# Kernel optimization log

Hardware: AMD Instinct MI355X
Metric: run time of the kernel (lower is better)

## Reference

```python
import jax, jax.numpy as jnp
import numpy as np

B, S = 2, 2048
NUM_HEADS, NUM_KV_HEADS, HEAD_DIM = 32, 8, 128
HIDDEN = NUM_HEADS * HEAD_DIM  # 4096
Q_SIZE = NUM_HEADS * HEAD_DIM
KV_SIZE = NUM_KV_HEADS * HEAD_DIM
ROPE_THETA = 100000.0
SCALE = HEAD_DIM ** -0.5


def setup_inputs() -> dict:
    key = jax.random.key(0)
    k1, k2, k3, k4, k5 = jax.random.split(key, 5)
    T = B * S
    return {
        "hidden_states": jax.random.normal(k1, (T, HIDDEN), jnp.float32) * 0.02,
        "positions": jnp.arange(T, dtype=jnp.int64) % S,  # per-sequence positions
        "w_qkv": jax.random.normal(k2, (HIDDEN, Q_SIZE + 2 * KV_SIZE), jnp.float32) * 0.02,
        "b_qkv": jax.random.normal(k3, (Q_SIZE + 2 * KV_SIZE,), jnp.float32) * 0.01,
        "w_o": jax.random.normal(k4, (Q_SIZE, HIDDEN), jnp.float32) * 0.02,
        "b_o": jax.random.normal(k5, (HIDDEN,), jnp.float32) * 0.01,
    }


def _rope_neox(x, positions):
    # x: [T, H, D]; neox style rotates the two halves of head_dim
    half = HEAD_DIM // 2
    inv_freq = 1.0 / (ROPE_THETA ** (jnp.arange(0, HEAD_DIM, 2, dtype=jnp.float32) / HEAD_DIM))
    freqs = positions.astype(jnp.float32)[:, None] * inv_freq[None, :]  # [T, D/2]
    cos = jnp.cos(freqs)[:, None, :]  # [T, 1, D/2]
    sin = jnp.sin(freqs)[:, None, :]
    x1, x2 = x[..., :half], x[..., half:]
    return jnp.concatenate([x1 * cos - x2 * sin, x2 * cos + x1 * sin], axis=-1)


def reference(hidden_states, positions, w_qkv, b_qkv, w_o, b_o):
    T = hidden_states.shape[0]
    qkv = hidden_states @ w_qkv + b_qkv  # [T, q+2kv]
    q = qkv[:, :Q_SIZE].reshape(T, NUM_HEADS, HEAD_DIM)
    k = qkv[:, Q_SIZE:Q_SIZE + KV_SIZE].reshape(T, NUM_KV_HEADS, HEAD_DIM)
    v = qkv[:, Q_SIZE + KV_SIZE:].reshape(T, NUM_KV_HEADS, HEAD_DIM)

    q = _rope_neox(q, positions)
    k = _rope_neox(k, positions)

    # reshape flattened tokens back to [B, S, ...] for causal self-attention
    q = q.reshape(B, S, NUM_HEADS, HEAD_DIM)
    k = k.reshape(B, S, NUM_KV_HEADS, HEAD_DIM)
    v = v.reshape(B, S, NUM_KV_HEADS, HEAD_DIM)

    # GQA: repeat kv heads to match query heads
    group = NUM_HEADS // NUM_KV_HEADS
    k = jnp.repeat(k, group, axis=2)  # [B, S, H, D]
    v = jnp.repeat(v, group, axis=2)

    scores = jnp.einsum("bqhd,bkhd->bhqk", q, k) * SCALE  # [B, H, S, S]
    causal = jnp.tril(jnp.ones((S, S), dtype=bool))
    scores = jnp.where(causal[None, None], scores, jnp.finfo(scores.dtype).min)
    probs = jax.nn.softmax(scores, axis=-1)
    attn = jnp.einsum("bhqk,bkhd->bqhd", probs, v)  # [B, S, H, D]

    attn = attn.reshape(T, Q_SIZE)
    return attn @ w_o + b_o  # [T, HIDDEN]
```

## Files before the change

kernel.cpp:

```cpp
#include <hip/hip_runtime.h>
#include <cstdint>
#include <math.h>

#define T_TOTAL 4096
#define S_LEN   2048
#define NH      32
#define NKV     8
#define HD      128
#define HIDDEN  4096
#define QSZ     4096
#define KVSZ    1024
#define QKV_N   6144
#define SCALE_F 0.08838834764831843f

typedef __bf16 bf16x8 __attribute__((ext_vector_type(8)));
typedef float  f32x4  __attribute__((ext_vector_type(4)));
typedef unsigned short u16;
typedef unsigned int   u32;
typedef u16 u16x8 __attribute__((ext_vector_type(8)));
typedef u16 u16x4 __attribute__((ext_vector_type(4)));

__device__ __forceinline__ u16 f2bf(float f) {
  u32 b = __float_as_uint(f);
  b += 0x7FFFu + ((b >> 16) & 1u);
  return (u16)(b >> 16);
}

__device__ __forceinline__ void async_copy16(const u16* g, u16* l) {
  __builtin_amdgcn_global_load_lds(
      (const __attribute__((address_space(1))) void*)(g),
      (__attribute__((address_space(3))) void*)(l), 16, 0, 0);
}

__global__ __launch_bounds__(256) void cast_bf16_kernel(const float4* __restrict__ in,
                                                        ushort4* __restrict__ out, int n4) {
  int i = blockIdx.x * 256 + threadIdx.x;
  if (i >= n4) return;
  float4 v = in[i];
  ushort4 o;
  o.x = f2bf(v.x); o.y = f2bf(v.y); o.z = f2bf(v.z); o.w = f2bf(v.w);
  out[i] = o;
}

__global__ __launch_bounds__(256) void transpose_cast_kernel(const float* __restrict__ in,
                                                             u16* __restrict__ out, int R, int C) {
  __shared__ float tile[32][33];
  int bx = blockIdx.x * 32;
  int by = blockIdx.y * 32;
  int tx = threadIdx.x & 31, ty = threadIdx.x >> 5;
  for (int i = ty; i < 32; i += 8)
    tile[i][tx] = in[(size_t)(by + i) * C + bx + tx];
  __syncthreads();
  for (int i = ty; i < 32; i += 8)
    out[(size_t)(bx + i) * R + by + tx] = f2bf(tile[tx][i]);
}

__global__ __launch_bounds__(512) void gemm_pipe_kernel(const u16* __restrict__ A,
                                                        const u16* __restrict__ Bt,
                                                        const float* __restrict__ bias,
                                                        float* __restrict__ C,
                                                        int M, int N, int K, int nbn) {
  __shared__ u16 lds[2][2][8192];
  const int tid  = threadIdx.x;
  const int lane = tid & 63, wave = tid >> 6;
  const int quad = lane >> 4, l16 = lane & 15;
  const int wm = (wave >> 2) * 128;
  const int wn = (wave & 3) * 64;

  const int cpx = gridDim.x >> 3;
  const int logical = (blockIdx.x & 7) * cpx + (blockIdx.x >> 3);
  const int bm = logical / nbn, bn = logical % nbn;

  const int trow = tid >> 2;
  const int gch  = ((tid & 3) ^ ((tid >> 3) & 3)) * 8;
  const u16* gA = A  + (size_t)(bm * 256 + trow) * K + gch;
  const u16* gB = Bt + (size_t)(bn * 256 + trow) * K + gch;
  const size_t eoff = (size_t)128 * K;

  const int NT = K >> 5;
#pragma unroll
  for (int pt = 0; pt < 2; ++pt) {
    int kt = pt * 32;
    async_copy16(gA + kt,        &lds[pt][0][tid * 8]);
    async_copy16(gA + eoff + kt, &lds[pt][0][4096 + tid * 8]);
    async_copy16(gB + kt,        &lds[pt][1][tid * 8]);
    async_copy16(gB + eoff + kt, &lds[pt][1][4096 + tid * 8]);
  }

  const int sw = (quad ^ ((l16 >> 1) & 3)) * 8;
  f32x4 acc[8][4] = {};
  for (int t = 0; t < NT; ++t) {
    if (t + 1 < NT) asm volatile("s_waitcnt vmcnt(4)" ::: "memory");
    else            asm volatile("s_waitcnt vmcnt(0)" ::: "memory");
    __builtin_amdgcn_s_barrier();

    const u16* sAt = lds[t & 1][0];
    const u16* sBt = lds[t & 1][1];
    bf16x8 af[8], bfr[4];
#pragma unroll
    for (int i = 0; i < 8; ++i)
      af[i] = *(const bf16x8*)&sAt[(wm + i * 16 + l16) * 32 + sw];
#pragma unroll
    for (int j = 0; j < 4; ++j)
      bfr[j] = *(const bf16x8*)&sBt[(wn + j * 16 + l16) * 32 + sw];
    asm volatile("s_waitcnt lgkmcnt(0)" ::: "memory");
    __builtin_amdgcn_s_barrier();

    if (t + 2 < NT) {
      int kt = (t + 2) * 32;
      async_copy16(gA + kt,        &lds[t & 1][0][tid * 8]);
      async_copy16(gA + eoff + kt, &lds[t & 1][0][4096 + tid * 8]);
      async_copy16(gB + kt,        &lds[t & 1][1][tid * 8]);
      async_copy16(gB + eoff + kt, &lds[t & 1][1][4096 + tid * 8]);
    }

    __builtin_amdgcn_s_setprio(1);
#pragma unroll
    for (int i = 0; i < 8; ++i)
#pragma unroll
      for (int j = 0; j < 4; ++j)
        acc[i][j] = __builtin_amdgcn_mfma_f32_16x16x32_bf16(af[i], bfr[j], acc[i][j], 0, 0, 0);
    __builtin_amdgcn_s_setprio(0);
  }

#pragma unroll
  for (int i = 0; i < 8; ++i) {
    int row0 = bm * 256 + wm + i * 16 + quad * 4;
#pragma unroll
    for (int j = 0; j < 4; ++j) {
      int col = bn * 256 + wn + j * 16 + l16;
      float bi = bias[col];
#pragma unroll
      for (int r = 0; r < 4; ++r)
        C[(size_t)(row0 + r) * N + col] = acc[i][j][r] + bi;
    }
  }
}

__global__ __launch_bounds__(256) void qk_rope_cast_kernel(const float* __restrict__ qkv,
                                                           const int* __restrict__ pos,
                                                           u16* __restrict__ Qb,
                                                           u16* __restrict__ Kb) {
  int idx = blockIdx.x * 256 + threadIdx.x;
  int t = idx / 2560;
  int rem = idx - t * 2560;
  int head = rem >> 6, i = rem & 63;
  int b = t >> 11, s = t & 2047;
  float p = (float)pos[t];
  float inv = exp2f(-(float)i * 0.25952563f);
  float f = p * inv;
  float sn, cs;
  sincosf(f, &sn, &cs);
  if (head < NH) {
    const float* src = qkv + (size_t)t * QKV_N + head * HD;
    float x1 = src[i], x2 = src[i + 64];
    u16* dst = Qb + (((size_t)(b * NH + head)) * S_LEN + s) * HD;
    dst[i]      = f2bf((x1 * cs - x2 * sn) * SCALE_F);
    dst[i + 64] = f2bf((x2 * cs + x1 * sn) * SCALE_F);
  } else {
    int kh = head - NH;
    const float* src = qkv + (size_t)t * QKV_N + QSZ + kh * HD;
    float x1 = src[i], x2 = src[i + 64];
    u16* dst = Kb + (((size_t)(b * NKV + kh)) * S_LEN + s) * HD;
    dst[i]      = f2bf(x1 * cs - x2 * sn);
    dst[i + 64] = f2bf(x2 * cs + x1 * sn);
  }
}

__global__ __launch_bounds__(256) void v_transpose_cast_kernel(const float* __restrict__ qkv,
                                                               u16* __restrict__ Vtb) {
  __shared__ float tile[32][33];
  int st = blockIdx.x * 32;
  int dt = blockIdx.y * 32;
  int bk = blockIdx.z;
  int b = bk >> 3, kvh = bk & 7;
  int tx = threadIdx.x & 31, ty = threadIdx.x >> 5;
  const float* src = qkv + (size_t)(b * S_LEN) * QKV_N + QSZ + KVSZ + kvh * HD;
  for (int i = ty; i < 32; i += 8)
    tile[i][tx] = src[(size_t)(st + i) * QKV_N + dt + tx];
  __syncthreads();
  u16* dst = Vtb + (size_t)bk * HD * S_LEN;
  for (int i = ty; i < 32; i += 8)
    dst[(size_t)(dt + i) * S_LEN + st + tx] = f2bf(tile[tx][i]);
}

__global__ __launch_bounds__(512) void flash_mfma_kernel(const u16* __restrict__ Qb,
                                                         const u16* __restrict__ Kb,
                                                         const u16* __restrict__ Vtb,
                                                         u16* __restrict__ attn) {
  const int qti = gridDim.x - 1 - blockIdx.x;
  const int h = blockIdx.y, b = blockIdx.z;
  const int kvh = h >> 2;
  const int tid = threadIdx.x;
  const int lane = tid & 63, wave = tid >> 6;
  const int quad = lane >> 4, l16 = lane & 15;

  __shared__ u16 smem[24576];
  u16* sK  = smem;
  u16* sVt = smem + 8192;
  u16* sPw = smem + 16384 + wave * 1024;

  bf16x8 qf[4];
  {
    const u16* qrow = Qb + (((size_t)(b * NH + h)) * S_LEN + (size_t)qti * 128 + wave * 16 + l16) * HD;
#pragma unroll
    for (int kc = 0; kc < 4; ++kc)
      qf[kc] = *(const bf16x8*)(qrow + kc * 32 + quad * 8);
  }

  f32x4 acc[8] = {};
  float m_r = -INFINITY;
  float l_r = 0.f;

  const u16* Kbase = Kb  + ((size_t)(b * NKV + kvh)) * S_LEN * HD;
  const u16* Vbase = Vtb + ((size_t)(b * NKV + kvh)) * HD * S_LEN;

  u16x8 kv[2], vv[2];
#pragma unroll
  for (int i = 0; i < 2; ++i) {
    int c = i * 512 + tid;
    kv[i] = *(const u16x8*)(Kbase + (size_t)(c >> 4) * HD + (c & 15) * 8);
    vv[i] = *(const u16x8*)(Vbase + (size_t)(c >> 3) * S_LEN + (c & 7) * 8);
  }

  const int nkt = 2 * qti + 2;
  const int lastkt = 2 * qti + (wave >> 2);

  for (int kt = 0; kt < nkt; ++kt) {
    __syncthreads();
#pragma unroll
    for (int i = 0; i < 2; ++i) {
      int c = i * 512 + tid;
      int kr = c >> 4;
      *(u16x8*)&sK[(kr * 128 + (c & 15) * 8) ^ ((kr & 7) << 3)] = kv[i];
      int vr = c >> 3;
      *(u16x8*)&sVt[(vr * 64 + (c & 7) * 8) ^ ((vr & 7) << 3)] = vv[i];
    }
    __syncthreads();

    if (kt + 1 < nkt) {
#pragma unroll
      for (int i = 0; i < 2; ++i) {
        int c = i * 512 + tid;
        kv[i] = *(const u16x8*)(Kbase + (size_t)((kt + 1) * 64 + (c >> 4)) * HD + (c & 15) * 8);
        vv[i] = *(const u16x8*)(Vbase + (size_t)(c >> 3) * S_LEN + (kt + 1) * 64 + (c & 7) * 8);
      }
    }

    if (kt > lastkt) continue;

    f32x4 s[4] = {};
#pragma unroll
    for (int kc = 0; kc < 4; ++kc) {
#pragma unroll
      for (int nb = 0; nb < 4; ++nb) {
        bf16x8 kf = *(const bf16x8*)&sK[((nb * 16 + l16) * 128 + kc * 32 + quad * 8) ^ ((l16 & 7) << 3)];
        s[nb] = __builtin_amdgcn_mfma_f32_16x16x32_bf16(kf, qf[kc], s[nb], 0, 0, 0);
      }
    }

    if (kt == lastkt) {
      int qg = qti * 128 + wave * 16 + l16;
      int k0 = kt * 64;
#pragma unroll
      for (int nb = 0; nb < 4; ++nb)
#pragma unroll
        for (int r = 0; r < 4; ++r)
          if (k0 + nb * 16 + quad * 4 + r > qg) s[nb][r] = -1e30f;
    }

    float mx = -1e30f;
#pragma unroll
    for (int nb = 0; nb < 4; ++nb)
#pragma unroll
      for (int r = 0; r < 4; ++r)
        mx = fmaxf(mx, s[nb][r]);
    float alpha = 1.f;
    if (!__all(mx - m_r <= 8.f)) {
      mx = fmaxf(mx, __shfl_xor(mx, 16));
      mx = fmaxf(mx, __shfl_xor(mx, 32));
      float mnew = fmaxf(m_r, mx);
      alpha = __expf(m_r - mnew);
      m_r = mnew;
#pragma unroll
      for (int db = 0; db < 8; ++db)
#pragma unroll
        for (int r = 0; r < 4; ++r)
          acc[db][r] *= alpha;
    }
    float rs = 0.f;
#pragma unroll
    for (int nb = 0; nb < 4; ++nb)
#pragma unroll
      for (int r = 0; r < 4; ++r) {
        float p = __expf(s[nb][r] - m_r);
        s[nb][r] = p;
        rs += p;
      }
    rs += __shfl_xor(rs, 16);
    rs += __shfl_xor(rs, 32);
    l_r = l_r * alpha + rs;

#pragma unroll
    for (int nb = 0; nb < 4; ++nb) {
      u16x4 pk;
#pragma unroll
      for (int r = 0; r < 4; ++r) pk[r] = f2bf(s[nb][r]);
      *(u16x4*)&sPw[(l16 * 64 + nb * 16 + quad * 4) ^ ((l16 & 7) << 3)] = pk;
    }

#pragma unroll
    for (int ch = 0; ch < 2; ++ch) {
      bf16x8 pf = *(const bf16x8*)&sPw[(l16 * 64 + ch * 32 + quad * 8) ^ ((l16 & 7) << 3)];
#pragma unroll
      for (int db = 0; db < 8; ++db) {
        bf16x8 vf = *(const bf16x8*)&sVt[((db * 16 + l16) * 64 + ch * 32 + quad * 8) ^ ((l16 & 7) << 3)];
        acc[db] = __builtin_amdgcn_mfma_f32_16x16x32_bf16(vf, pf, acc[db], 0, 0, 0);
      }
    }
  }

  float invl = 1.0f / l_r;
  __syncthreads();
  u16* sOw = &smem[wave * 2048];
#pragma unroll
  for (int db = 0; db < 8; ++db) {
    u16x4 pk;
#pragma unroll
    for (int r = 0; r < 4; ++r) pk[r] = f2bf(acc[db][r] * invl);
    *(u16x4*)&sOw[(l16 * 128 + db * 16 + quad * 4) ^ ((l16 & 7) << 3)] = pk;
  }
#pragma unroll
  for (int p = 0; p < 4; ++p) {
    int row = p * 4 + quad;
    u16x8 o = *(const u16x8*)&sOw[(row * 128 + l16 * 8) ^ ((row & 7) << 3)];
    int q = qti * 128 + wave * 16 + row;
    *(u16x8*)(attn + ((size_t)(b * S_LEN + q)) * QSZ + (size_t)h * HD + l16 * 8) = o;
  }
}

extern "C" void kernel_launch(void* const* d_in, const int* in_sizes, int n_in,
                              void* d_out, int out_size, void* d_ws, size_t ws_size,
                              hipStream_t stream) {
  const float* hidden    = (const float*)d_in[0];
  const int*   positions = (const int*)d_in[1];
  const float* w_qkv     = (const float*)d_in[2];
  const float* b_qkv     = (const float*)d_in[3];
  const float* w_o       = (const float*)d_in[4];
  const float* b_o       = (const float*)d_in[5];
  float* out = (float*)d_out;

  char* ws = (char*)d_ws;
  const size_t MB = 1024 * 1024;
  u16*   hb    = (u16*)ws;
  u16*   wqT   = (u16*)(ws + 32  * MB);
  u16*   woT   = (u16*)(ws + 80  * MB);
  float* qkv   = (float*)(ws + 112 * MB);
  u16*   attnb = (u16*)(ws + 208 * MB);
  u16*   Qb    = (u16*)ws;
  u16*   Kb    = (u16*)(ws + 32 * MB);
  u16*   Vtb   = (u16*)(ws + 40 * MB);

  cast_bf16_kernel<<<T_TOTAL * HIDDEN / 4 / 256, 256, 0, stream>>>(
      (const float4*)hidden, (ushort4*)hb, T_TOTAL * HIDDEN / 4);
  transpose_cast_kernel<<<dim3(QKV_N / 32, HIDDEN / 32), 256, 0, stream>>>(w_qkv, wqT, HIDDEN, QKV_N);
  transpose_cast_kernel<<<dim3(HIDDEN / 32, QSZ / 32), 256, 0, stream>>>(w_o, woT, QSZ, HIDDEN);
  gemm_pipe_kernel<<<dim3((T_TOTAL / 256) * (QKV_N / 256)), 512, 0, stream>>>(
      hb, wqT, b_qkv, qkv, T_TOTAL, QKV_N, HIDDEN, QKV_N / 256);
  qk_rope_cast_kernel<<<T_TOTAL * 2560 / 256, 256, 0, stream>>>(qkv, positions, Qb, Kb);
  v_transpose_cast_kernel<<<dim3(S_LEN / 32, HD / 32, 16), 256, 0, stream>>>(qkv, Vtb);
  flash_mfma_kernel<<<dim3(S_LEN / 128, NH, 2), 512, 0, stream>>>(Qb, Kb, Vtb, attnb);
  gemm_pipe_kernel<<<dim3((T_TOTAL / 256) * (HIDDEN / 256)), 512, 0, stream>>>(
      attnb, woT, b_o, out, T_TOTAL, HIDDEN, QSZ, HIDDEN / 256);
}
```

Baseline: 887.7 us.

## Shrink GEMM M-tile to 128 and use triple-buffered LDS with single barrier

The GEMM block tile goes from 256x256 to 128x256, which doubles the number of blocks so more CUs get work (the QKV GEMM had 384 blocks and the output GEMM 256). LDS is now a three-stage ring, so the prefetch for tile t+2 can be issued right after the first barrier, and the second per-iteration barrier is removed. In exchange, arithmetic intensity per block is lower because each B tile is reused for half as many rows, so L2 and global traffic go up.

Measured after the change: 887.6 us. No clear change (-0.0%).

```diff
diff --git a/kernel.cpp b/kernel.cpp
--- a/kernel.cpp
+++ b/kernel.cpp
@@ -60,72 +60,72 @@
                                                         const float* __restrict__ bias,
                                                         float* __restrict__ C,
                                                         int M, int N, int K, int nbn) {
-  __shared__ u16 lds[2][2][8192];
+  __shared__ u16 lds[3][12288];
   const int tid  = threadIdx.x;
   const int lane = tid & 63, wave = tid >> 6;
   const int quad = lane >> 4, l16 = lane & 15;
-  const int wm = (wave >> 2) * 128;
+  const int wm = (wave >> 2) * 64;
   const int wn = (wave & 3) * 64;
 
   const int cpx = gridDim.x >> 3;
   const int logical = (blockIdx.x & 7) * cpx + (blockIdx.x >> 3);
   const int bm = logical / nbn, bn = logical % nbn;
 
-  const int trow = tid >> 2;
-  const int gch  = ((tid & 3) ^ ((tid >> 3) & 3)) * 8;
-  const u16* gA = A  + (size_t)(bm * 256 + trow) * K + gch;
-  const u16* gB = Bt + (size_t)(bn * 256 + trow) * K + gch;
-  const size_t eoff = (size_t)128 * K;
+  const int gch = ((tid & 3) ^ ((tid >> 3) & 3)) * 8;
+  const u16* gA  = A  + (size_t)(bm * 128 + (tid >> 2)) * K + gch;
+  const u16* gB0 = Bt + (size_t)(bn * 256 + (tid >> 2)) * K + gch;
+  const u16* gB1 = gB0 + (size_t)128 * K;
 
   const int NT = K >> 5;
 #pragma unroll
   for (int pt = 0; pt < 2; ++pt) {
     int kt = pt * 32;
-    async_copy16(gA + kt,        &lds[pt][0][tid * 8]);
-    async_copy16(gA + eoff + kt, &lds[pt][0][4096 + tid * 8]);
-    async_copy16(gB + kt,        &lds[pt][1][tid * 8]);
-    async_copy16(gB + eoff + kt, &lds[pt][1][4096 + tid * 8]);
+    async_copy16(gA  + kt, &lds[pt][tid * 8]);
+    async_copy16(gB0 + kt, &lds[pt][4096 + tid * 8]);
+    async_copy16(gB1 + kt, &lds[pt][8192 + tid * 8]);
   }
 
   const int sw = (quad ^ ((l16 >> 1) & 3)) * 8;
-  f32x4 acc[8][4] = {};
+  f32x4 acc[4][4] = {};
+  int sl = 0;
   for (int t = 0; t < NT; ++t) {
-    if (t + 1 < NT) asm volatile("s_waitcnt vmcnt(4)" ::: "memory");
+    if (t + 1 < NT) asm volatile("s_waitcnt vmcnt(3)" ::: "memory");
     else            asm volatile("s_waitcnt vmcnt(0)" ::: "memory");
     __builtin_amdgcn_s_barrier();
 
-    const u16* sAt = lds[t & 1][0];
-    const u16* sBt = lds[t & 1][1];
-    bf16x8 af[8], bfr[4];
-#pragma unroll
-    for (int i = 0; i < 8; ++i)
+    int s2 = (sl == 0) ? 2 : sl - 1;
+    if (t + 2 < NT) {
+      int kt = (t + 2) * 32;
+      async_copy16(gA  + kt, &lds[s2][tid * 8]);
+      async_copy16(gB0 + kt, &lds[s2][4096 + tid * 8]);
+      async_copy16(gB1 + kt, &lds[s2][8192 + tid * 8]);
+    }
+
+    const u16* sAt = lds[sl];
+    const u16* sBt = &lds[sl][4096];
+    bf16x8 af[4], bfr[4];
+#pragma unroll
+    for (int i = 0; i < 4; ++i)
       af[i] = *(const bf16x8*)&sAt[(wm + i * 16 + l16) * 32 + sw];
 #pragma unroll
     for (int j = 0; j < 4; ++j)
       bfr[j] = *(const bf16x8*)&sBt[(wn + j * 16 + l16) * 32 + sw];
     asm volatile("s_waitcnt lgkmcnt(0)" ::: "memory");
-    __builtin_amdgcn_s_barrier();
-
-    if (t + 2 < NT) {
-      int kt = (t + 2) * 32;
-      async_copy16(gA + kt,        &lds[t & 1][0][tid * 8]);
-      async_copy16(gA + eoff + kt, &lds[t & 1][0][4096 + tid * 8]);
-      async_copy16(gB + kt,        &lds[t & 1][1][tid * 8]);
-      async_copy16(gB + eoff + kt, &lds[t & 1][1][4096 + tid * 8]);
-    }
 
     __builtin_amdgcn_s_setprio(1);
 #pragma unroll
-    for (int i = 0; i < 8; ++i)
+    for (int i = 0; i < 4; ++i)
 #pragma unroll
       for (int j = 0; j < 4; ++j)
         acc[i][j] = __builtin_amdgcn_mfma_f32_16x16x32_bf16(af[i], bfr[j], acc[i][j], 0, 0, 0);
     __builtin_amdgcn_s_setprio(0);
-  }
-
-#pragma unroll
-  for (int i = 0; i < 8; ++i) {
-    int row0 = bm * 256 + wm + i * 16 + quad * 4;
+
+    sl = (sl == 2) ? 0 : sl + 1;
+  }
+
+#pragma unroll
+  for (int i = 0; i < 4; ++i) {
+    int row0 = bm * 128 + wm + i * 16 + quad * 4;
 #pragma unroll
     for (int j = 0; j < 4; ++j) {
       int col = bn * 256 + wn + j * 16 + l16;
@@ -365,11 +365,11 @@
       (const float4*)hidden, (ushort4*)hb, T_TOTAL * HIDDEN / 4);
   transpose_cast_kernel<<<dim3(QKV_N / 32, HIDDEN / 32), 256, 0, stream>>>(w_qkv, wqT, HIDDEN, QKV_N);
   transpose_cast_kernel<<<dim3(HIDDEN / 32, QSZ / 32), 256, 0, stream>>>(w_o, woT, QSZ, HIDDEN);
-  gemm_pipe_kernel<<<dim3((T_TOTAL / 256) * (QKV_N / 256)), 512, 0, stream>>>(
+  gemm_pipe_kernel<<<dim3((T_TOTAL / 128) * (QKV_N / 256)), 512, 0, stream>>>(
       hb, wqT, b_qkv, qkv, T_TOTAL, QKV_N, HIDDEN, QKV_N / 256);
   qk_rope_cast_kernel<<<T_TOTAL * 2560 / 256, 256, 0, stream>>>(qkv, positions, Qb, Kb);
   v_transpose_cast_kernel<<<dim3(S_LEN / 32, HD / 32, 16), 256, 0, stream>>>(qkv, Vtb);
   flash_mfma_kernel<<<dim3(S_LEN / 128, NH, 2), 512, 0, stream>>>(Qb, Kb, Vtb, attnb);
-  gemm_pipe_kernel<<<dim3((T_TOTAL / 256) * (HIDDEN / 256)), 512, 0, stream>>>(
+  gemm_pipe_kernel<<<dim3((T_TOTAL / 128) * (HIDDEN / 256)), 512, 0, stream>>>(
       attnb, woT, b_o, out, T_TOTAL, HIDDEN, QSZ, HIDDEN / 256);
 }
```
